# Kernel tuning notes

Hardware: AMD Instinct MI355X
Metric: run time of the kernel (lower is better)

The kernel has to match this reference:

```python
import jax, jax.numpy as jnp
import numpy as np


def conv_gates(x, w, b):
    # x: [B, L, Din]; w: [3O, Din, k]; torch Conv1d with padding=(k-1)//2
    xt = jnp.transpose(x, (0, 2, 1))  # [B, Din, L]
    pad = (w.shape[-1] - 1) // 2
    g = jax.lax.conv_general_dilated(
        xt, w, window_strides=(1,), padding=[(pad, pad)],
        dimension_numbers=('NCH', 'OIH', 'NCH')) + b[None, :, None]
    g = jnp.transpose(g, (0, 2, 1))  # [B, L, 3O]
    f, o, z = jnp.split(g, 3, axis=-1)
    return jax.nn.sigmoid(f), jax.nn.sigmoid(o), jnp.tanh(z)


def fo_pool(f, z):
    # f, z: [B, L, O]; cell_t = f_t * cell_{t-1} + (1 - f_t) * z_t, cell_{-1}=0
    def step(c, fz):
        ft, zt = fz
        c = ft * c + (1.0 - ft) * zt
        return c, c
    c0 = jnp.zeros((f.shape[0], f.shape[2]), f.dtype)
    _, cells = jax.lax.scan(step, c0, (jnp.swapaxes(f, 0, 1), jnp.swapaxes(z, 0, 1)))
    return jnp.swapaxes(cells, 0, 1)  # [B, L, O]


def qrnn_layer(x, wf, bf, wr, br):
    # forward direction
    f, o, z = conv_gates(x, wf, bf)
    cells = fo_pool(f, z)
    hidden = cells * o
    # reverse direction: run recurrence on time-flipped gates, flip back
    fr, orr, zr = conv_gates(x, wr, br)
    rcells = fo_pool(fr[:, ::-1], zr[:, ::-1])[:, ::-1]
    rhidden = rcells * orr
    out = jnp.concatenate([hidden, rhidden], -1)  # [B, L, 2O]
    last_h = jnp.concatenate([hidden[:, -1], rhidden[:, -1]], -1)  # [B, 2O]
    last_c = jnp.concatenate([cells[:, -1], rcells[:, -1]], -1)
    return out, last_h, last_c


def setup_inputs() -> dict:
    key = jax.random.key(0)
    ks = jax.random.split(key, 9)
    D, O, K = 512, 512, 3
    B, L = 16, 2048
    s = 0.05
    return {
        'x': jax.random.normal(ks[0], (B, L, D), jnp.float32),
        'w0f': jax.random.normal(ks[1], (3 * O, D, K), jnp.float32) * s,
        'b0f': jax.random.normal(ks[2], (3 * O,), jnp.float32) * s,
        'w0r': jax.random.normal(ks[3], (3 * O, D, K), jnp.float32) * s,
        'b0r': jax.random.normal(ks[4], (3 * O,), jnp.float32) * s,
        'w1f': jax.random.normal(ks[5], (3 * O, 2 * O, K), jnp.float32) * s,
        'b1f': jax.random.normal(ks[6], (3 * O,), jnp.float32) * s,
        'w1r': jax.random.normal(ks[7], (3 * O, 2 * O, K), jnp.float32) * s,
        'b1r': jax.random.normal(ks[8], (3 * O,), jnp.float32) * s,
    }


def reference(x, w0f, b0f, w0r, b0r, w1f, b1f, w1r, b1r):
    out1, h1, c1 = qrnn_layer(x, w0f, b0f, w0r, b0r)
    out2, h2, c2 = qrnn_layer(out1, w1f, b1f, w1r, b1r)
    B = x.shape[0]
    O = h1.shape[-1] // 2
    # torch: cat along dim 0 -> [2B, 2O] then view(num_dir*num_layers, B, O)
    hidden = jnp.concatenate([h1, h2], 0).reshape(4, B, O)
    cell = jnp.concatenate([c1, c2], 0).reshape(4, B, O)
    return out2, hidden, cell
```

## Files before the change

kernel.cpp:

```cpp
#include <hip/hip_runtime.h>

typedef _Float16 f16x8 __attribute__((ext_vector_type(8)));
typedef float    f32x4 __attribute__((ext_vector_type(4)));

#define GLDS16(gp, lp) \
  __builtin_amdgcn_global_load_lds((const __attribute__((address_space(1))) void*)(gp), \
                                   (__attribute__((address_space(3))) void*)(lp), 16, 0, 0)

#define NB   16
#define LL   2048
#define LP   2050
#define C3   1536
#define OO   512

__global__ void cvt_x_kernel(const float* __restrict__ x, _Float16* __restrict__ xp) {
  int t = blockIdx.x * blockDim.x + threadIdx.x;
  const int total = NB * LP * (512 / 8);
  if (t >= total) return;
  int c8  = (t & 63) << 3;
  int row = t >> 6;
  int b   = row / LP;
  int lp  = row - b * LP;
  f16x8 v;
  if (lp == 0 || lp == LP - 1) {
#pragma unroll
    for (int i = 0; i < 8; ++i) v[i] = (_Float16)0.f;
  } else {
    const float* s = x + ((size_t)(b * LL + lp - 1) * 512 + c8);
    const float4* s4 = (const float4*)s;
    float4 a = s4[0], bq = s4[1];
    v[0] = (_Float16)a.x;  v[1] = (_Float16)a.y;
    v[2] = (_Float16)a.z;  v[3] = (_Float16)a.w;
    v[4] = (_Float16)bq.x; v[5] = (_Float16)bq.y;
    v[6] = (_Float16)bq.z; v[7] = (_Float16)bq.w;
  }
  *(f16x8*)(xp + (size_t)row * 512 + c8) = v;
}

__global__ void cvt_w_kernel(const float* __restrict__ w, _Float16* __restrict__ wt,
                             int Din, int dinsh) {
  int t = blockIdx.x * blockDim.x + threadIdx.x;
  if (t >= C3 * Din) return;
  int c = t >> dinsh;
  int i = t & (Din - 1);
  const float* s = w + (size_t)t * 3;
  wt[((size_t)c * 3 + 0) * Din + i] = (_Float16)s[0];
  wt[((size_t)c * 3 + 1) * Din + i] = (_Float16)s[1];
  wt[((size_t)c * 3 + 2) * Din + i] = (_Float16)s[2];
}

__global__ void zero_pad_kernel(_Float16* __restrict__ xp1) {
  int t = blockIdx.x * blockDim.x + threadIdx.x;
  if (t >= NB * 2 * 1024) return;
  int col = t & 1023;
  int r   = (t >> 10) & 1;
  int b   = t >> 11;
  xp1[((size_t)b * LP + (r ? (LP - 1) : 0)) * 1024 + col] = (_Float16)0.f;
}

__global__ __launch_bounds__(256) void conv_gemm(
    const _Float16* __restrict__ A, const _Float16* __restrict__ W,
    const float* __restrict__ bias, _Float16* __restrict__ G, int Din)
{
  const int nT = blockIdx.x, lT = blockIdx.y, b = blockIdx.z;
  const int tid  = (int)threadIdx.x;
  const int w    = tid >> 6, lane = tid & 63;
  const int wr   = w >> 1,   wc   = w & 1;
  const int l0   = lT << 7,  n0   = nT << 7;

  __shared__ _Float16 Als[132 * 32];
  __shared__ _Float16 Bls[3 * 128 * 32];

  f32x4 acc[4][4];
  const f32x4 zed = {0.f, 0.f, 0.f, 0.f};
#pragma unroll
  for (int i = 0; i < 4; ++i)
#pragma unroll
    for (int j = 0; j < 4; ++j) acc[i][j] = zed;

  const int rl   = lane >> 2;
  const int kswz = ((lane & 3) ^ (rl & 3)) << 3;
  const _Float16* Ab = A + ((size_t)(b * LP + l0)) * Din;

  const int rA = lane & 15;
  const int kq = lane >> 4;

  for (int kt = 0; kt < Din; kt += 32) {
    __syncthreads();
#pragma unroll
    for (int j = 0; j < 2; ++j) {
      const int chunk = w + (j << 2);
      const int row   = (chunk << 4) + rl;
      GLDS16(Ab + (size_t)row * Din + (kt + kswz), (char*)Als + (chunk << 10));
    }
    if (w == 0 && lane < 8) {
      const int row = 128 + rl;
      GLDS16(Ab + (size_t)row * Din + (kt + kswz), (char*)Als + (8 << 10));
    }
#pragma unroll
    for (int j = 0; j < 6; ++j) {
      const int chunkid = w * 6 + j;
      const int tap     = chunkid >> 3;
      const int row     = ((chunkid & 7) << 4) + rl;
      GLDS16(W + ((size_t)((n0 + row) * 3 + tap)) * Din + (kt + kswz),
             (char*)Bls + (chunkid << 10));
    }
    __syncthreads();

#pragma unroll
    for (int tap = 0; tap < 3; ++tap) {
      f16x8 af[4], bf[4];
#pragma unroll
      for (int i = 0; i < 4; ++i) {
        const int ra = wr * 64 + i * 16 + rA + tap;
        const int rb = wc * 64 + i * 16 + rA;
        af[i] = *(const f16x8*)((const char*)Als + (ra << 6) + ((kq ^ (ra & 3)) << 4));
        bf[i] = *(const f16x8*)((const char*)Bls + (tap << 13) + (rb << 6) + ((kq ^ (rb & 3)) << 4));
      }
#pragma unroll
      for (int mi = 0; mi < 4; ++mi)
#pragma unroll
        for (int ni = 0; ni < 4; ++ni)
          acc[mi][ni] = __builtin_amdgcn_mfma_f32_16x16x32_f16(af[mi], bf[ni], acc[mi][ni], 0, 0, 0);
    }
  }

#pragma unroll
  for (int ni = 0; ni < 4; ++ni) {
    const int col = n0 + wc * 64 + ni * 16 + (lane & 15);
    const float bv = bias[col];
#pragma unroll
    for (int mi = 0; mi < 4; ++mi) {
#pragma unroll
      for (int r = 0; r < 4; ++r) {
        const int l = l0 + wr * 64 + mi * 16 + ((lane >> 4) << 2) + r;
        float v = acc[mi][ni][r] + bv;
        v = fminf(fmaxf(v, -30.f), 30.f);
        float a;
        if (col < 1024) {
          a = 1.f / (1.f + __expf(-v));
        } else {
          float e = __expf(2.f * v);
          a = (e - 1.f) / (e + 1.f);
        }
        G[((size_t)(b * LL + l)) * C3 + col] = (_Float16)a;
      }
    }
  }
}

__global__ void fo_phase1(const _Float16* __restrict__ g, float* __restrict__ P,
                          float* __restrict__ S, int dir) {
  int t = blockIdx.x * blockDim.x + threadIdx.x;
  if (t >= 32 * 8192) return;
  int bo = t & 8191;
  int ch = t >> 13;
  int b = bo >> 9, o = bo & 511;
  float c = 0.f, p = 1.f;
  const int s0 = ch * 64;
  for (int k = 0; k < 64; ++k) {
    int s = s0 + k;
    int l = dir ? (2047 - s) : s;
    size_t base = ((size_t)(b * LL + l)) * C3 + o;
    float f = (float)g[base];
    float z = (float)g[base + 1024];
    c = f * c + (1.f - f) * z;
    p *= f;
  }
  P[t] = p;
  S[t] = c;
}

__global__ void fo_phase2(const float* __restrict__ P, const float* __restrict__ S,
                          float* __restrict__ cst) {
  int bo = blockIdx.x * blockDim.x + threadIdx.x;
  if (bo >= 8192) return;
  float c = 0.f;
#pragma unroll
  for (int j = 0; j < 32; ++j) {
    cst[j * 8192 + bo] = c;
    c = P[j * 8192 + bo] * c + S[j * 8192 + bo];
  }
}

__global__ void fo_phase3(const _Float16* __restrict__ g, const float* __restrict__ cst,
                          int dir, int layer, _Float16* __restrict__ nxt,
                          float* __restrict__ out2, float* __restrict__ hc) {
  int t = blockIdx.x * blockDim.x + threadIdx.x;
  if (t >= 32 * 8192) return;
  int bo = t & 8191;
  int ch = t >> 13;
  int b = bo >> 9, o = bo & 511;
  float c = cst[t];
  const int s0 = ch * 64;
  for (int k = 0; k < 64; ++k) {
    int s = s0 + k;
    int l = dir ? (2047 - s) : s;
    size_t base = ((size_t)(b * LL + l)) * C3 + o;
    float f  = (float)g[base];
    float og = (float)g[base + 512];
    float z  = (float)g[base + 1024];
    c = f * c + (1.f - f) * z;
    float h = c * og;
    if (layer == 0)
      nxt[((size_t)(b * LP + l + 1)) * 1024 + dir * 512 + o] = (_Float16)h;
    else
      out2[((size_t)(b * LL + l)) * 1024 + dir * 512 + o] = h;
    if (l == 2047) {
      hc[(layer * 16 + b) * 1024 + dir * 512 + o] = h;
      hc[32768 + (layer * 16 + b) * 1024 + dir * 512 + o] = c;
    }
  }
}

extern "C" void kernel_launch(void* const* d_in, const int* in_sizes, int n_in,
                              void* d_out, int out_size, void* d_ws, size_t ws_size,
                              hipStream_t stream) {
  const float* x   = (const float*)d_in[0];
  const float* w0f = (const float*)d_in[1];
  const float* b0f = (const float*)d_in[2];
  const float* w0r = (const float*)d_in[3];
  const float* b0r = (const float*)d_in[4];
  const float* w1f = (const float*)d_in[5];
  const float* b1f = (const float*)d_in[6];
  const float* w1r = (const float*)d_in[7];
  const float* b1r = (const float*)d_in[8];
  float* out = (float*)d_out;

  char* ws = (char*)d_ws;
  _Float16* xp0  = (_Float16*)(ws + 0);
  _Float16* xp1  = (_Float16*)(ws + 33587200);
  _Float16* wt0f = (_Float16*)(ws + 100761600);
  _Float16* wt0r = (_Float16*)(ws + 105480192);
  _Float16* wt1f = (_Float16*)(ws + 110198784);
  _Float16* wt1r = (_Float16*)(ws + 119635968);
  _Float16* g    = (_Float16*)(ws + 129073152);
  float*    P    = (float*)(ws + 229736448);
  float*    S    = (float*)(ws + 230785024);
  float*    cst  = (float*)(ws + 231833600);

  float* hc = out + (size_t)16 * 2048 * 1024;

  cvt_x_kernel<<<8200, 256, 0, stream>>>(x, xp0);
  cvt_w_kernel<<<3072, 256, 0, stream>>>(w0f, wt0f, 512, 9);
  cvt_w_kernel<<<3072, 256, 0, stream>>>(w0r, wt0r, 512, 9);
  cvt_w_kernel<<<6144, 256, 0, stream>>>(w1f, wt1f, 1024, 10);
  cvt_w_kernel<<<6144, 256, 0, stream>>>(w1r, wt1r, 1024, 10);
  zero_pad_kernel<<<128, 256, 0, stream>>>(xp1);

  dim3 gg(12, 16, 16);

  conv_gemm<<<gg, 256, 0, stream>>>(xp0, wt0f, b0f, g, 512);
  fo_phase1<<<1024, 256, 0, stream>>>(g, P, S, 0);
  fo_phase2<<<32, 256, 0, stream>>>(P, S, cst);
  fo_phase3<<<1024, 256, 0, stream>>>(g, cst, 0, 0, xp1, out, hc);
  conv_gemm<<<gg, 256, 0, stream>>>(xp0, wt0r, b0r, g, 512);
  fo_phase1<<<1024, 256, 0, stream>>>(g, P, S, 1);
  fo_phase2<<<32, 256, 0, stream>>>(P, S, cst);
  fo_phase3<<<1024, 256, 0, stream>>>(g, cst, 1, 0, xp1, out, hc);
  conv_gemm<<<gg, 256, 0, stream>>>(xp1, wt1f, b1f, g, 1024);
  fo_phase1<<<1024, 256, 0, stream>>>(g, P, S, 0);
  fo_phase2<<<32, 256, 0, stream>>>(P, S, cst);
  fo_phase3<<<1024, 256, 0, stream>>>(g, cst, 0, 1, xp1, out, hc);
  conv_gemm<<<gg, 256, 0, stream>>>(xp1, wt1r, b1r, g, 1024);
  fo_phase1<<<1024, 256, 0, stream>>>(g, P, S, 1);
  fo_phase2<<<32, 256, 0, stream>>>(P, S, cst);
  fo_phase3<<<1024, 256, 0, stream>>>(g, cst, 1, 1, xp1, out, hc);
}
```

Baseline: 1.426 ms.

## Remap conv GEMM blocks per XCD, relayout LDS tiles, stage epilogue through LDS

The conv GEMM grid is flattened to 1D and block indices are remapped so that the 12 N-tiles sharing one A tile land on the same XCD, which should improve L2 reuse of activations. The LDS layout for A and B changes from a row-swizzled form to a k-quarter-major chunk layout that matches the MFMA fragment reads. The epilogue now writes activated gates into a padded LDS tile and then stores 16-byte vectors to global memory, replacing scattered 2-byte stores. The cost is extra shared memory (about 34 KB) and two more barriers, and LDS bank conflicts may change with the new layout.

Result: slower. 1.590 ms (+11.5%).

```diff
diff --git a/kernel.cpp b/kernel.cpp
--- a/kernel.cpp
+++ b/kernel.cpp
@@ -62,14 +62,22 @@
     const _Float16* __restrict__ A, const _Float16* __restrict__ W,
     const float* __restrict__ bias, _Float16* __restrict__ G, int Din)
 {
-  const int nT = blockIdx.x, lT = blockIdx.y, b = blockIdx.z;
+  const int bid  = (int)blockIdx.x;
+  const int xcd  = bid & 7, slot = bid >> 3;
+  const int grp  = (slot / 12) * 8 + xcd;
+  const int nT   = slot % 12;
+  const int lT   = grp & 15, b = grp >> 4;
+
   const int tid  = (int)threadIdx.x;
   const int w    = tid >> 6, lane = tid & 63;
   const int wr   = w >> 1,   wc   = w & 1;
   const int l0   = lT << 7,  n0   = nT << 7;
-
-  __shared__ _Float16 Als[132 * 32];
-  __shared__ _Float16 Bls[3 * 128 * 32];
+  const int rA   = lane & 15;
+  const int kq   = lane >> 4;
+
+  __shared__ _Float16 smem[17408];
+  _Float16* Als = smem;
+  _Float16* Bls = smem + 4608;
 
   f32x4 acc[4][4];
   const f32x4 zed = {0.f, 0.f, 0.f, 0.f};
@@ -78,31 +86,27 @@
 #pragma unroll
     for (int j = 0; j < 4; ++j) acc[i][j] = zed;
 
-  const int rl   = lane >> 2;
-  const int kswz = ((lane & 3) ^ (rl & 3)) << 3;
   const _Float16* Ab = A + ((size_t)(b * LP + l0)) * Din;
-
-  const int rA = lane & 15;
-  const int kq = lane >> 4;
+  const int srcK = kq << 3;
 
   for (int kt = 0; kt < Din; kt += 32) {
     __syncthreads();
 #pragma unroll
     for (int j = 0; j < 2; ++j) {
       const int chunk = w + (j << 2);
-      const int row   = (chunk << 4) + rl;
-      GLDS16(Ab + (size_t)row * Din + (kt + kswz), (char*)Als + (chunk << 10));
-    }
-    if (w == 0 && lane < 8) {
-      const int row = 128 + rl;
-      GLDS16(Ab + (size_t)row * Din + (kt + kswz), (char*)Als + (8 << 10));
+      GLDS16(Ab + (size_t)((chunk << 4) + rA) * Din + (kt + srcK),
+             (char*)Als + (chunk << 10));
+    }
+    if (w == 3 && rA < 2) {
+      GLDS16(Ab + (size_t)(128 + rA) * Din + (kt + srcK),
+             (char*)Als + (8 << 10));
     }
 #pragma unroll
     for (int j = 0; j < 6; ++j) {
       const int chunkid = w * 6 + j;
       const int tap     = chunkid >> 3;
-      const int row     = ((chunkid & 7) << 4) + rl;
-      GLDS16(W + ((size_t)((n0 + row) * 3 + tap)) * Din + (kt + kswz),
+      const int c       = chunkid & 7;
+      GLDS16(W + ((size_t)((n0 + (c << 4) + rA) * 3 + tap)) * Din + (kt + srcK),
              (char*)Bls + (chunkid << 10));
     }
     __syncthreads();
@@ -112,10 +116,11 @@
       f16x8 af[4], bf[4];
 #pragma unroll
       for (int i = 0; i < 4; ++i) {
-        const int ra = wr * 64 + i * 16 + rA + tap;
-        const int rb = wc * 64 + i * 16 + rA;
-        af[i] = *(const f16x8*)((const char*)Als + (ra << 6) + ((kq ^ (ra & 3)) << 4));
-        bf[i] = *(const f16x8*)((const char*)Bls + (tap << 13) + (rb << 6) + ((kq ^ (rb & 3)) << 4));
+        const int r = wr * 64 + i * 16 + rA + tap;
+        af[i] = *(const f16x8*)((const char*)Als +
+                 ((r >> 4) << 10) + ((((kq << 4) + (r & 15))) << 4));
+        bf[i] = *(const f16x8*)((const char*)Bls +
+                 (tap << 13) + (((wc << 2) + i) << 10) + (lane << 4));
       }
 #pragma unroll
       for (int mi = 0; mi < 4; ++mi)
@@ -125,27 +130,38 @@
     }
   }
 
+  __syncthreads();
+  _Float16* T = smem;
 #pragma unroll
   for (int ni = 0; ni < 4; ++ni) {
-    const int col = n0 + wc * 64 + ni * 16 + (lane & 15);
-    const float bv = bias[col];
+    const int col = wc * 64 + ni * 16 + rA;
+    const float bv = bias[n0 + col];
 #pragma unroll
     for (int mi = 0; mi < 4; ++mi) {
 #pragma unroll
       for (int r = 0; r < 4; ++r) {
-        const int l = l0 + wr * 64 + mi * 16 + ((lane >> 4) << 2) + r;
+        const int row = wr * 64 + mi * 16 + (kq << 2) + r;
         float v = acc[mi][ni][r] + bv;
         v = fminf(fmaxf(v, -30.f), 30.f);
         float a;
-        if (col < 1024) {
+        if (n0 + col < 1024) {
           a = 1.f / (1.f + __expf(-v));
         } else {
           float e = __expf(2.f * v);
           a = (e - 1.f) / (e + 1.f);
         }
-        G[((size_t)(b * LL + l)) * C3 + col] = (_Float16)a;
+        T[row * 136 + col] = (_Float16)a;
       }
     }
+  }
+  __syncthreads();
+  _Float16* Gb = G + ((size_t)(b * LL + l0)) * C3 + n0;
+#pragma unroll
+  for (int p = 0; p < 8; ++p) {
+    const int row = (p << 4) + (tid >> 4);
+    const int cc  = (tid & 15) << 3;
+    f16x8 v = *(const f16x8*)(T + row * 136 + cc);
+    *(f16x8*)(Gb + (size_t)row * C3 + cc) = v;
   }
 }
 
@@ -248,21 +264,19 @@
   cvt_w_kernel<<<6144, 256, 0, stream>>>(w1r, wt1r, 1024, 10);
   zero_pad_kernel<<<128, 256, 0, stream>>>(xp1);
 
-  dim3 gg(12, 16, 16);
-
-  conv_gemm<<<gg, 256, 0, stream>>>(xp0, wt0f, b0f, g, 512);
+  conv_gemm<<<3072, 256, 0, stream>>>(xp0, wt0f, b0f, g, 512);
   fo_phase1<<<1024, 256, 0, stream>>>(g, P, S, 0);
   fo_phase2<<<32, 256, 0, stream>>>(P, S, cst);
   fo_phase3<<<1024, 256, 0, stream>>>(g, cst, 0, 0, xp1, out, hc);
-  conv_gemm<<<gg, 256, 0, stream>>>(xp0, wt0r, b0r, g, 512);
+  conv_gemm<<<3072, 256, 0, stream>>>(xp0, wt0r, b0r, g, 512);
   fo_phase1<<<1024, 256, 0, stream>>>(g, P, S, 1);
   fo_phase2<<<32, 256, 0, stream>>>(P, S, cst);
   fo_phase3<<<1024, 256, 0, stream>>>(g, cst, 1, 0, xp1, out, hc);
-  conv_gemm<<<gg, 256, 0, stream>>>(xp1, wt1f, b1f, g, 1024);
+  conv_gemm<<<3072, 256, 0, stream>>>(xp1, wt1f, b1f, g, 1024);
   fo_phase1<<<1024, 256, 0, stream>>>(g, P, S, 0);
   fo_phase2<<<32, 256, 0, stream>>>(P, S, cst);
   fo_phase3<<<1024, 256, 0, stream>>>(g, cst, 0, 1, xp1, out, hc);
-  conv_gemm<<<gg, 256, 0, stream>>>(xp1, wt1r, b1r, g, 1024);
+  conv_gemm<<<3072, 256, 0, stream>>>(xp1, wt1r, b1r, g, 1024);
   fo_phase1<<<1024, 256, 0, stream>>>(g, P, S, 1);
   fo_phase2<<<32, 256, 0, stream>>>(P, S, cst);
   fo_phase3<<<1024, 256, 0, stream>>>(g, cst, 1, 1, xp1, out, hc);
```
